# Kernel tuning notes

Hardware: AMD Instinct MI355X
Metric: run time of the kernel (lower is better)

The kernel has to match this reference:

```python
import jax, jax.numpy as jnp
import numpy as np

N, E, G = 50000, 800000, 64
IN, H, C = 128, 3, 64
HC = H * C


def _conv(x, src, dst, Wq, bq, Wk, bk, Wv, bv, Ws, bs, Wb):
    # node-level projections, then per-edge gather
    q = (x @ Wq + bq).reshape(-1, H, C)[dst]   # [E,H,C]
    k = (x @ Wk + bk).reshape(-1, H, C)[src]
    v = (x @ Wv + bv).reshape(-1, H, C)[src]
    alpha = (q * k).sum(-1) / jnp.sqrt(jnp.float32(C))  # [E,H]
    # segment softmax over incoming edges of each target node
    amax = jax.ops.segment_max(alpha, dst, num_segments=N)
    amax = jnp.where(jnp.isfinite(amax), amax, 0.0)
    ex = jnp.exp(alpha - amax[dst])
    denom = jax.ops.segment_sum(ex, dst, num_segments=N)
    a = ex / (denom[dst] + 1e-16)
    out = jax.ops.segment_sum(a[:, :, None] * v, dst, num_segments=N).reshape(-1, HC)
    # gated skip (beta=True, root_weight=True)
    r = x @ Ws + bs
    beta = jax.nn.sigmoid(jnp.concatenate([out, r, out - r], -1) @ Wb)  # [N,1]
    return beta * r + (1.0 - beta) * out


def setup_inputs() -> dict:
    key = jax.random.key(0)
    ks = jax.random.split(key, 32)
    x = jax.random.normal(ks[0], (N, IN), dtype=jnp.float32)
    edge_index = jax.random.randint(ks[1], (2, E), 0, N, dtype=jnp.int32)
    batch = jnp.sort(jax.random.randint(ks[2], (N,), 0, G, dtype=jnp.int32))
    s = 0.05
    def w(k, shape):
        return jax.random.normal(k, shape, dtype=jnp.float32) * s
    d = {"x": x, "edge_index": edge_index, "batch": batch}
    ins = [IN, HC]
    ki = 3
    for l in range(2):
        din = ins[l]
        d[f"Wq{l}"] = w(ks[ki], (din, HC)); ki += 1
        d[f"bq{l}"] = jnp.zeros((HC,), jnp.float32)
        d[f"Wk{l}"] = w(ks[ki], (din, HC)); ki += 1
        d[f"bk{l}"] = jnp.zeros((HC,), jnp.float32)
        d[f"Wv{l}"] = w(ks[ki], (din, HC)); ki += 1
        d[f"bv{l}"] = jnp.zeros((HC,), jnp.float32)
        d[f"Ws{l}"] = w(ks[ki], (din, HC)); ki += 1
        d[f"bs{l}"] = jnp.zeros((HC,), jnp.float32)
        d[f"Wb{l}"] = w(ks[ki], (3 * HC, 1)); ki += 1
    d["Wlin"] = w(ks[ki], (HC, 1)); ki += 1
    d["blin"] = jnp.zeros((1,), jnp.float32)
    return d


def reference(x, edge_index, batch,
              Wq0, bq0, Wk0, bk0, Wv0, bv0, Ws0, bs0, Wb0,
              Wq1, bq1, Wk1, bk1, Wv1, bv1, Ws1, bs1, Wb1,
              Wlin, blin):
    src, dst = edge_index[0], edge_index[1]
    h = _conv(x, src, dst, Wq0, bq0, Wk0, bk0, Wv0, bv0, Ws0, bs0, Wb0)
    h = jax.nn.elu(h)
    h = _conv(h, src, dst, Wq1, bq1, Wk1, bk1, Wv1, bv1, Ws1, bs1, Wb1)
    h = jax.nn.elu(h)
    # global mean pool over graphs
    cnt = jax.ops.segment_sum(jnp.ones((N,), jnp.float32), batch, num_segments=G)
    pooled = jax.ops.segment_sum(h, batch, num_segments=G) / jnp.maximum(cnt, 1.0)[:, None]
    logits = (pooled @ Wlin + blin).squeeze(-1)  # [G]
    return logits
```

## Files before the change

kernel.cpp:

```cpp
#include <hip/hip_runtime.h>
#include <math.h>

#define NNODES 50000
#define NEDGES 800000
#define NGRAPH 64
#define DIM_IN 128
#define HCDIM  192
#define QKVRW  768

typedef __attribute__((ext_vector_type(8))) short short8;
typedef __attribute__((ext_vector_type(4))) float f32x4;
typedef __attribute__((ext_vector_type(2))) float f32x2;

__device__ __forceinline__ unsigned short f2bf(float f){
  unsigned int u = __float_as_uint(f);
  unsigned int r = (u + 0x7fffu + ((u>>16)&1u)) >> 16;
  return (unsigned short)r;
}

__device__ __forceinline__ float4 bf4_to_f4(uint2 u){
  float4 f;
  f.x = __uint_as_float(u.x<<16);
  f.y = __uint_as_float(u.x & 0xffff0000u);
  f.z = __uint_as_float(u.y<<16);
  f.w = __uint_as_float(u.y & 0xffff0000u);
  return f;
}

__device__ __forceinline__ float4 fp8x4_to_f4(unsigned int u){
  f32x2 lo = __builtin_amdgcn_cvt_pk_f32_fp8((int)u, false);
  f32x2 hi = __builtin_amdgcn_cvt_pk_f32_fp8((int)u, true);
  float4 f; f.x=lo[0]; f.y=lo[1]; f.z=hi[0]; f.w=hi[1];
  return f;
}

__device__ __forceinline__ float wave_sum(float v){
#pragma unroll
  for(int off=32; off>0; off>>=1) v += __shfl_xor(v, off, 64);
  return v;
}

__global__ void zero2_k(int* a, int* b, int n){
  int i = blockIdx.x*blockDim.x + threadIdx.x;
  if(i<n){ a[i]=0; b[i]=0; }
}

__global__ void hist_k(const int* __restrict__ dst, int* __restrict__ counts, int E){
  int e = blockIdx.x*blockDim.x + threadIdx.x;
  if(e<E) atomicAdd(&counts[dst[e]], 1);
}

__global__ void scan_partial(const int* __restrict__ counts, int* __restrict__ bsum, int N){
  __shared__ int lds[256];
  int t = threadIdx.x;
  int idx = blockIdx.x*256 + t;
  int v = (idx<N)? counts[idx] : 0;
  lds[t]=v; __syncthreads();
#pragma unroll
  for(int off=128; off>0; off>>=1){
    if(t<off) lds[t]+=lds[t+off];
    __syncthreads();
  }
  if(t==0) bsum[blockIdx.x]=lds[0];
}

__global__ void scan_bsum(int* bsum, int nb){
  __shared__ int lds[1024];
  int t=threadIdx.x;
  int v=(t<nb)?bsum[t]:0;
  lds[t]=v; __syncthreads();
  int x=v;
#pragma unroll
  for(int off=1; off<1024; off<<=1){
    int y=(t>=off)?lds[t-off]:0;
    __syncthreads();
    x+=y; lds[t]=x;
    __syncthreads();
  }
  if(t<nb) bsum[t]=x-v;
}

__global__ void scan_final(const int* __restrict__ counts, const int* __restrict__ bsum,
                           int* __restrict__ row_ptr, int N){
  __shared__ int lds[256];
  int t=threadIdx.x;
  int idx=blockIdx.x*256+t;
  int v=(idx<N)?counts[idx]:0;
  lds[t]=v; __syncthreads();
  int x=v;
#pragma unroll
  for(int off=1; off<256; off<<=1){
    int y=(t>=off)?lds[t-off]:0;
    __syncthreads();
    x+=y; lds[t]=x;
    __syncthreads();
  }
  if(idx<=N) row_ptr[idx]= bsum[blockIdx.x]+x-v;
}

__global__ void fill_k(const int* __restrict__ src, const int* __restrict__ dst,
                       const int* __restrict__ row_ptr, int* __restrict__ cursor,
                       int* __restrict__ csr_src, int E){
  int e = blockIdx.x*blockDim.x + threadIdx.x;
  if(e<E){
    int d = dst[e];
    int pos = row_ptr[d] + atomicAdd(&cursor[d], 1);
    csr_src[pos] = src[e];
  }
}

#define CAST_BLKS (NNODES*DIM_IN/4/256)
__global__ void prep0_k(const float* __restrict__ X, unsigned short* __restrict__ Xb,
                        const float* __restrict__ Wq, const float* __restrict__ Wk,
                        const float* __restrict__ Wv, const float* __restrict__ Ws,
                        const float* __restrict__ bq, const float* __restrict__ bk,
                        const float* __restrict__ bv, const float* __restrict__ bs,
                        unsigned short* __restrict__ Wt, float* __restrict__ bcat){
  if(blockIdx.x < CAST_BLKS){
    int i4 = (blockIdx.x*256 + threadIdx.x)*4;
    float4 v = *(const float4*)(X+i4);
    ushort4 o; o.x=f2bf(v.x); o.y=f2bf(v.y); o.z=f2bf(v.z); o.w=f2bf(v.w);
    *(ushort4*)(Xb+i4) = o;
  } else {
    int idx = (blockIdx.x-CAST_BLKS)*256 + threadIdx.x;
    if(idx < QKVRW*DIM_IN){
      int c = idx / DIM_IN, k = idx % DIM_IN;
      int mat = c/HCDIM, cm = c%HCDIM;
      const float* W = (mat==0)?Wq:(mat==1)?Wk:(mat==2)?Wv:Ws;
      Wt[(size_t)c*DIM_IN + k] = f2bf(W[(size_t)k*HCDIM + cm]);
    }
    if(idx < QKVRW){
      int mat = idx/HCDIM, cm = idx%HCDIM;
      const float* b = (mat==0)?bq:(mat==1)?bk:(mat==2)?bv:bs;
      bcat[idx] = b[cm];
    }
  }
}

__global__ void build_wt(const float* __restrict__ Wq, const float* __restrict__ Wk,
                         const float* __restrict__ Wv, const float* __restrict__ Ws,
                         const float* __restrict__ bq, const float* __restrict__ bk,
                         const float* __restrict__ bv, const float* __restrict__ bs,
                         unsigned short* __restrict__ Wt, float* __restrict__ bcat, int K){
  int idx = blockIdx.x*256 + threadIdx.x;
  if(idx < QKVRW*K){
    int c = idx / K, k = idx % K;
    int mat = c/HCDIM, cm = c%HCDIM;
    const float* W = (mat==0)?Wq:(mat==1)?Wk:(mat==2)?Wv:Ws;
    Wt[(size_t)c*K + k] = f2bf(W[(size_t)k*HCDIM + cm]);
  }
  if(idx < QKVRW){
    int mat = idx/HCDIM, cm = idx%HCDIM;
    const float* b = (mat==0)?bq:(mat==1)?bk:(mat==2)?bv:bs;
    bcat[idx] = b[cm];
  }
}

template<int K>
__global__ __launch_bounds__(256) void gemm_mfma(
    const unsigned short* __restrict__ Xb,
    const unsigned short* __restrict__ Wt,
    const float* __restrict__ bcat,
    unsigned short* __restrict__ QR,
    unsigned char* __restrict__ KV, int N)
{
  __shared__ unsigned short As[128*64];
  __shared__ unsigned short Bs[64*64];
  const int tid = threadIdx.x;
  const int wv = tid>>6;
  const int lane = tid&63;
  const int m0  = blockIdx.x*128;
  const int cb  = blockIdx.y;
  const int mat = cb/3;
  const int nc0 = cb*64;

  const int wr = wv>>1, wc = wv&1;
  const int lhi = lane>>4, llo = lane&15;
  f32x4 acc[4][2] = {};

  constexpr int NT = K/64;
#pragma unroll
  for(int kt=0; kt<NT; ++kt){
    if(kt>0) __syncthreads();
#pragma unroll
    for(int it=0; it<4; ++it){
      int p = it*256 + tid;
      int r = p>>3, c = p&7;
      int cs = c ^ (r&7);
      int grow = m0 + r; if(grow > N-1) grow = N-1;
      const unsigned short* gp = Xb + (size_t)grow*K + kt*64 + cs*8;
      unsigned short* lp = As + (size_t)(it*256 + wv*64)*8;
      __builtin_amdgcn_global_load_lds(
          (const __attribute__((address_space(1))) unsigned int*)gp,
          (__attribute__((address_space(3))) unsigned int*)lp, 16, 0, 0);
    }
#pragma unroll
    for(int it=0; it<2; ++it){
      int p = it*256 + tid;
      int r = p>>3, c = p&7;
      int cs = c ^ (r&7);
      const unsigned short* gp = Wt + (size_t)(nc0 + r)*K + kt*64 + cs*8;
      unsigned short* lp = Bs + (size_t)(it*256 + wv*64)*8;
      __builtin_amdgcn_global_load_lds(
          (const __attribute__((address_space(1))) unsigned int*)gp,
          (__attribute__((address_space(3))) unsigned int*)lp, 16, 0, 0);
    }
    __syncthreads();

#pragma unroll
    for(int kk=0; kk<64; kk+=32){
      short8 a[4], b[2];
      const int chunk = (kk>>3) + lhi;
#pragma unroll
      for(int i=0;i<4;++i){
        int rr = wr*64 + i*16 + llo;
        int cs = chunk ^ (rr&7);
        a[i] = *(const short8*)(As + rr*64 + cs*8);
      }
#pragma unroll
      for(int j=0;j<2;++j){
        int cc = wc*32 + j*16 + llo;
        int cs = chunk ^ (cc&7);
        b[j] = *(const short8*)(Bs + cc*64 + cs*8);
      }
#pragma unroll
      for(int i=0;i<4;++i)
#pragma unroll
        for(int j=0;j<2;++j)
          acc[i][j] = __builtin_amdgcn_mfma_f32_16x16x32_bf16(a[i], b[j], acc[i][j], 0,0,0);
    }
  }

  const int col0 = nc0 + wc*32 + llo;
  float bias0 = bcat[col0];
  float bias1 = bcat[col0+16];
  if(mat==0 || mat==3){
    const int coff = (mat==0) ? col0 : col0-384;
#pragma unroll
    for(int i=0;i<4;++i){
#pragma unroll
      for(int r=0;r<4;++r){
        int grow = m0 + wr*64 + i*16 + lhi*4 + r;
        if(grow < N){
          size_t base = (size_t)grow*384 + coff;
          QR[base]      = f2bf(acc[i][0][r] + bias0);
          QR[base + 16] = f2bf(acc[i][1][r] + bias1);
        }
      }
    }
  } else {
#pragma unroll
    for(int i=0;i<4;++i){
#pragma unroll
      for(int r=0;r<4;++r){
        int grow = m0 + wr*64 + i*16 + lhi*4 + r;
        float v0 = acc[i][0][r] + bias0;
        float v1 = acc[i][1][r] + bias1;
        float n0 = __shfl_xor(v0, 1, 64);
        float n1 = __shfl_xor(v1, 1, 64);
        if(((llo&1)==0) && grow < N){
          int p0 = __builtin_amdgcn_cvt_pk_fp8_f32(v0, n0, 0, false);
          int p1 = __builtin_amdgcn_cvt_pk_fp8_f32(v1, n1, 0, false);
          unsigned char* kb = KV + (size_t)grow*384 + (col0-192);
          *(unsigned short*)(kb)    = (unsigned short)(p0 & 0xffff);
          *(unsigned short*)(kb+16) = (unsigned short)(p1 & 0xffff);
        }
      }
    }
  }
}

template<bool OUTBF>
__global__ __launch_bounds__(256) void attn_kernel(
  const unsigned short* __restrict__ QR,
  const unsigned char* __restrict__ KV,
  const int* __restrict__ row_ptr, const int* __restrict__ csr_src,
  const float* __restrict__ Wb, float* __restrict__ HoutF,
  unsigned short* __restrict__ HoutB, int N)
{
  const int wave = threadIdx.x>>6;
  const int lane = threadIdx.x&63;
  const int g    = lane>>4;
  const int l    = lane&15;
  const int n = blockIdx.x*4 + wave;
  if(n>=N) return;

  const unsigned short* nr = QR + (size_t)n*384 + 4*l;
  float4 q0 = bf4_to_f4(*(const uint2*)(nr));
  float4 q1 = bf4_to_f4(*(const uint2*)(nr+64));
  float4 q2 = bf4_to_f4(*(const uint2*)(nr+128));

  const int s0 = row_ptr[n];
  const int deg = row_ptr[n+1]-s0;

  float4 a0={0,0,0,0}, a1={0,0,0,0}, a2={0,0,0,0};
  float d0=0.f,d1=0.f,d2=0.f;

  unsigned int ku0=0,ku1=0,ku2=0,vu0=0,vu1=0,vu2=0;
  if(deg>0){
    int i0 = s0 + (g<deg ? g : 0); if(i0 > NEDGES-1) i0 = NEDGES-1;
    int sCur = csr_src[i0];
    const unsigned int* kv = (const unsigned int*)(KV + (size_t)sCur*384) + l;
    ku0=kv[0]; ku1=kv[16]; ku2=kv[32]; vu0=kv[48]; vu1=kv[64]; vu2=kv[80];
  }
  for(int base=0; base<deg; base+=4){
    const int inext = base + 4 + g;
    const int sNxt = csr_src[s0 + (inext<deg ? inext : 0)];
    const unsigned int* kvN = (const unsigned int*)(KV + (size_t)sNxt*384) + l;
    unsigned int nk0=kvN[0], nk1=kvN[16], nk2=kvN[32];
    unsigned int nv0=kvN[48], nv1=kvN[64], nv2=kvN[80];

    const bool valid = (base + g < deg);
    float4 k0 = fp8x4_to_f4(ku0);
    float4 k1 = fp8x4_to_f4(ku1);
    float4 k2 = fp8x4_to_f4(ku2);
    float p0 = q0.x*k0.x+q0.y*k0.y+q0.z*k0.z+q0.w*k0.w;
    float p1 = q1.x*k1.x+q1.y*k1.y+q1.z*k1.z+q1.w*k1.w;
    float p2 = q2.x*k2.x+q2.y*k2.y+q2.z*k2.z+q2.w*k2.w;
#pragma unroll
    for(int off=1; off<16; off<<=1){
      p0 += __shfl_xor(p0, off, 64);
      p1 += __shfl_xor(p1, off, 64);
      p2 += __shfl_xor(p2, off, 64);
    }
    float e0 = valid ? __expf(0.125f*p0) : 0.f;
    float e1 = valid ? __expf(0.125f*p1) : 0.f;
    float e2 = valid ? __expf(0.125f*p2) : 0.f;
    d0 += e0; d1 += e1; d2 += e2;
    float4 v0 = fp8x4_to_f4(vu0);
    float4 v1 = fp8x4_to_f4(vu1);
    float4 v2 = fp8x4_to_f4(vu2);
    a0.x+=e0*v0.x; a0.y+=e0*v0.y; a0.z+=e0*v0.z; a0.w+=e0*v0.w;
    a1.x+=e1*v1.x; a1.y+=e1*v1.y; a1.z+=e1*v1.z; a1.w+=e1*v1.w;
    a2.x+=e2*v2.x; a2.y+=e2*v2.y; a2.z+=e2*v2.z; a2.w+=e2*v2.w;

    ku0=nk0; ku1=nk1; ku2=nk2; vu0=nv0; vu1=nv1; vu2=nv2;
  }

#pragma unroll
  for(int off=16; off<64; off<<=1){
    a0.x+=__shfl_xor(a0.x,off,64); a0.y+=__shfl_xor(a0.y,off,64);
    a0.z+=__shfl_xor(a0.z,off,64); a0.w+=__shfl_xor(a0.w,off,64);
    a1.x+=__shfl_xor(a1.x,off,64); a1.y+=__shfl_xor(a1.y,off,64);
    a1.z+=__shfl_xor(a1.z,off,64); a1.w+=__shfl_xor(a1.w,off,64);
    a2.x+=__shfl_xor(a2.x,off,64); a2.y+=__shfl_xor(a2.y,off,64);
    a2.z+=__shfl_xor(a2.z,off,64); a2.w+=__shfl_xor(a2.w,off,64);
    d0+=__shfl_xor(d0,off,64); d1+=__shfl_xor(d1,off,64); d2+=__shfl_xor(d2,off,64);
  }
  const float id0=1.f/(d0+1e-16f), id1=1.f/(d1+1e-16f), id2=1.f/(d2+1e-16f);
  float4 o0, o1, o2;
  o0.x=a0.x*id0; o0.y=a0.y*id0; o0.z=a0.z*id0; o0.w=a0.w*id0;
  o1.x=a1.x*id1; o1.y=a1.y*id1; o1.z=a1.z*id1; o1.w=a1.w*id1;
  o2.x=a2.x*id2; o2.y=a2.y*id2; o2.z=a2.z*id2; o2.w=a2.w*id2;

  float4 r0 = bf4_to_f4(*(const uint2*)(nr+192));
  float4 r1 = bf4_to_f4(*(const uint2*)(nr+256));
  float4 r2 = bf4_to_f4(*(const uint2*)(nr+320));

  const float* wb = Wb + 4*l;
  float4 w00=*(const float4*)(wb),     w01=*(const float4*)(wb+64),  w02=*(const float4*)(wb+128);
  float4 w10=*(const float4*)(wb+192), w11=*(const float4*)(wb+256), w12=*(const float4*)(wb+320);
  float4 w20=*(const float4*)(wb+384), w21=*(const float4*)(wb+448), w22=*(const float4*)(wb+512);
  float z =
    o0.x*w00.x+o0.y*w00.y+o0.z*w00.z+o0.w*w00.w +
    o1.x*w01.x+o1.y*w01.y+o1.z*w01.z+o1.w*w01.w +
    o2.x*w02.x+o2.y*w02.y+o2.z*w02.z+o2.w*w02.w +
    r0.x*w10.x+r0.y*w10.y+r0.z*w10.z+r0.w*w10.w +
    r1.x*w11.x+r1.y*w11.y+r1.z*w11.z+r1.w*w11.w +
    r2.x*w12.x+r2.y*w12.y+r2.z*w12.z+r2.w*w12.w +
    (o0.x-r0.x)*w20.x+(o0.y-r0.y)*w20.y+(o0.z-r0.z)*w20.z+(o0.w-r0.w)*w20.w +
    (o1.x-r1.x)*w21.x+(o1.y-r1.y)*w21.y+(o1.z-r1.z)*w21.z+(o1.w-r1.w)*w21.w +
    (o2.x-r2.x)*w22.x+(o2.y-r2.y)*w22.y+(o2.z-r2.z)*w22.z+(o2.w-r2.w)*w22.w;
#pragma unroll
  for(int off=1; off<16; off<<=1) z += __shfl_xor(z, off, 64);
  const float beta = 1.f/(1.f+__expf(-z));
  float4 h0,h1,h2;
  h0.x=beta*r0.x+(1.f-beta)*o0.x; h0.y=beta*r0.y+(1.f-beta)*o0.y;
  h0.z=beta*r0.z+(1.f-beta)*o0.z; h0.w=beta*r0.w+(1.f-beta)*o0.w;
  h1.x=beta*r1.x+(1.f-beta)*o1.x; h1.y=beta*r1.y+(1.f-beta)*o1.y;
  h1.z=beta*r1.z+(1.f-beta)*o1.z; h1.w=beta*r1.w+(1.f-beta)*o1.w;
  h2.x=beta*r2.x+(1.f-beta)*o2.x; h2.y=beta*r2.y+(1.f-beta)*o2.y;
  h2.z=beta*r2.z+(1.f-beta)*o2.z; h2.w=beta*r2.w+(1.f-beta)*o2.w;
  h0.x=(h0.x>0.f)?h0.x:expm1f(h0.x); h0.y=(h0.y>0.f)?h0.y:expm1f(h0.y);
  h0.z=(h0.z>0.f)?h0.z:expm1f(h0.z); h0.w=(h0.w>0.f)?h0.w:expm1f(h0.w);
  h1.x=(h1.x>0.f)?h1.x:expm1f(h1.x); h1.y=(h1.y>0.f)?h1.y:expm1f(h1.y);
  h1.z=(h1.z>0.f)?h1.z:expm1f(h1.z); h1.w=(h1.w>0.f)?h1.w:expm1f(h1.w);
  h2.x=(h2.x>0.f)?h2.x:expm1f(h2.x); h2.y=(h2.y>0.f)?h2.y:expm1f(h2.y);
  h2.z=(h2.z>0.f)?h2.z:expm1f(h2.z); h2.w=(h2.w>0.f)?h2.w:expm1f(h2.w);
  if(g==0){
    if(OUTBF){
      unsigned short* hb = HoutB + (size_t)n*HCDIM + 4*l;
      ushort4 u0, u1, u2;
      u0.x=f2bf(h0.x); u0.y=f2bf(h0.y); u0.z=f2bf(h0.z); u0.w=f2bf(h0.w);
      u1.x=f2bf(h1.x); u1.y=f2bf(h1.y); u1.z=f2bf(h1.z); u1.w=f2bf(h1.w);
      u2.x=f2bf(h2.x); u2.y=f2bf(h2.y); u2.z=f2bf(h2.z); u2.w=f2bf(h2.w);
      *(ushort4*)(hb)     = u0;
      *(ushort4*)(hb+64)  = u1;
      *(ushort4*)(hb+128) = u2;
    } else {
      float* ho = HoutF + (size_t)n*HCDIM + 4*l;
      *(float4*)(ho)     = h0;
      *(float4*)(ho+64)  = h1;
      *(float4*)(ho+128) = h2;
    }
  }
}

__global__ void zero_pool(float* pooled, int* cnt){
  int i = blockIdx.x*256 + threadIdx.x;
  if(i < NGRAPH*HCDIM) ((int*)pooled)[i]=0;
  if(i < NGRAPH) cnt[i]=0;
}

__global__ void pool_k(const float* __restrict__ H, const int* __restrict__ batch,
                       float* __restrict__ pooled, int* __restrict__ cnt, int N){
  const int t = threadIdx.x;
  int start = blockIdx.x*256;
  int end = min(start+256, N);
  if(start>=N) return;
  int cur = batch[start];
  float acc = 0.f;
  int run = 0;
  for(int nn=start; nn<end; ++nn){
    int g = batch[nn];
    if(g!=cur){
      atomicAdd(&pooled[(size_t)cur*HCDIM+t], acc);
      if(t==0) atomicAdd(&cnt[cur], run);
      acc=0.f; run=0; cur=g;
    }
    acc += H[(size_t)nn*HCDIM+t];
    run++;
  }
  atomicAdd(&pooled[(size_t)cur*HCDIM+t], acc);
  if(t==0) atomicAdd(&cnt[cur], run);
}

__global__ void logits_k(const float* __restrict__ pooled, const int* __restrict__ cnt,
                         const float* __restrict__ Wlin, const float* __restrict__ blin,
                         float* __restrict__ out){
  const int g = blockIdx.x;
  const int lane = threadIdx.x;
  float c = fmaxf((float)cnt[g], 1.f);
  float s = 0.f;
#pragma unroll
  for(int j=0;j<3;++j){
    int col = j*64+lane;
    s += pooled[(size_t)g*HCDIM+col]/c * Wlin[col];
  }
  s = wave_sum(s);
  if(lane==0) out[g] = s + blin[0];
}

extern "C" void kernel_launch(void* const* d_in, const int* in_sizes, int n_in,
                              void* d_out, int out_size, void* d_ws, size_t ws_size,
                              hipStream_t stream)
{
  const int N=NNODES, E=NEDGES;
  const float* x     = (const float*)d_in[0];
  const int*   ei    = (const int*)d_in[1];
  const int*   batch = (const int*)d_in[2];
  const int* esrc = ei;
  const int* edst = ei + E;
  const float* Wq0=(const float*)d_in[3];  const float* bq0=(const float*)d_in[4];
  const float* Wk0=(const float*)d_in[5];  const float* bk0=(const float*)d_in[6];
  const float* Wv0=(const float*)d_in[7];  const float* bv0=(const float*)d_in[8];
  const float* Ws0=(const float*)d_in[9];  const float* bs0=(const float*)d_in[10];
  const float* Wb0=(const float*)d_in[11];
  const float* Wq1=(const float*)d_in[12]; const float* bq1=(const float*)d_in[13];
  const float* Wk1=(const float*)d_in[14]; const float* bk1=(const float*)d_in[15];
  const float* Wv1=(const float*)d_in[16]; const float* bv1=(const float*)d_in[17];
  const float* Ws1=(const float*)d_in[18]; const float* bs1=(const float*)d_in[19];
  const float* Wb1=(const float*)d_in[20];
  const float* Wlin=(const float*)d_in[21];
  const float* blin=(const float*)d_in[22];
  float* out = (float*)d_out;

  char* p = (char*)d_ws;
  auto alloc = [&](size_t bytes)->char*{
    char* q = p; p += (bytes+255)/256*256; return q;
  };
  unsigned short* Xb   = (unsigned short*)alloc((size_t)N*HCDIM*2);
  unsigned short* QR   = (unsigned short*)alloc((size_t)N*384*2);
  unsigned char*  KV   = (unsigned char*)alloc((size_t)N*384);
  float* H1            = (float*)alloc((size_t)N*HCDIM*4);
  unsigned short* Wt   = (unsigned short*)alloc((size_t)QKVRW*HCDIM*2);
  float* bcat          = (float*)alloc(QKVRW*4);
  int* counts  = (int*)alloc((size_t)N*4);
  int* cursor  = (int*)alloc((size_t)N*4);
  int* row_ptr = (int*)alloc((size_t)(N+1)*4);
  int* csr     = (int*)alloc((size_t)E*4);
  int* bsum    = (int*)alloc(4096);
  float* pooled= (float*)alloc((size_t)NGRAPH*HCDIM*4);
  int* cnt     = (int*)alloc(256);

  const int NB = (N+255)/256;

  zero2_k<<<(N+255)/256,256,0,stream>>>(counts,cursor,N);
  hist_k<<<(E+255)/256,256,0,stream>>>(edst,counts,E);
  scan_partial<<<NB,256,0,stream>>>(counts,bsum,N);
  scan_bsum<<<1,1024,0,stream>>>(bsum,NB);
  scan_final<<<NB,256,0,stream>>>(counts,bsum,row_ptr,N);
  fill_k<<<(E+255)/256,256,0,stream>>>(esrc,edst,row_ptr,cursor,csr,E);

  dim3 ggemm((N+127)/128, 12);
  prep0_k<<<CAST_BLKS + (QKVRW*DIM_IN+255)/256, 256, 0, stream>>>(
      x, Xb, Wq0,Wk0,Wv0,Ws0, bq0,bk0,bv0,bs0, Wt, bcat);
  gemm_mfma<DIM_IN><<<ggemm,256,0,stream>>>(Xb,Wt,bcat,QR,KV,N);
  attn_kernel<true><<<(N+3)/4,256,0,stream>>>(QR,KV,row_ptr,csr,Wb0,nullptr,Xb,N);
  build_wt<<<(QKVRW*HCDIM+255)/256,256,0,stream>>>(Wq1,Wk1,Wv1,Ws1,bq1,bk1,bv1,bs1,Wt,bcat,HCDIM);
  gemm_mfma<HCDIM><<<ggemm,256,0,stream>>>(Xb,Wt,bcat,QR,KV,N);
  attn_kernel<false><<<(N+3)/4,256,0,stream>>>(QR,KV,row_ptr,csr,Wb1,H1,nullptr,N);

  zero_pool<<<(NGRAPH*HCDIM+255)/256,256,0,stream>>>(pooled,cnt);
  pool_k<<<(N+255)/256,192,0,stream>>>(H1,batch,pooled,cnt,N);
  logits_k<<<NGRAPH,64,0,stream>>>(pooled,cnt,Wlin,blin,out);
}
```

Before: 406.1 us.

## Widen GEMM column tile to 128 and reorder weight blocks Q,S,K,V

The fused QKVS projection GEMM now computes 128x128 output tiles instead of 128x64, halving the grid's column dimension and doubling per-wave accumulators. This halves re-reads of the activation tile per output. Weight and bias blocks are reordered to Q,S,K,V so each 128-column tile writes either only the bf16 Q/R buffer or only the fp8 K/V buffer. The cost is more registers and LDS per block, which may lower occupancy, plus fewer blocks to spread across the GPU.

After: 408.5 us. No clear change (+0.6%).

```diff
diff --git a/kernel.cpp b/kernel.cpp
--- a/kernel.cpp
+++ b/kernel.cpp
@@ -126,12 +126,12 @@
     if(idx < QKVRW*DIM_IN){
       int c = idx / DIM_IN, k = idx % DIM_IN;
       int mat = c/HCDIM, cm = c%HCDIM;
-      const float* W = (mat==0)?Wq:(mat==1)?Wk:(mat==2)?Wv:Ws;
+      const float* W = (mat==0)?Wq:(mat==1)?Ws:(mat==2)?Wk:Wv;
       Wt[(size_t)c*DIM_IN + k] = f2bf(W[(size_t)k*HCDIM + cm]);
     }
     if(idx < QKVRW){
       int mat = idx/HCDIM, cm = idx%HCDIM;
-      const float* b = (mat==0)?bq:(mat==1)?bk:(mat==2)?bv:bs;
+      const float* b = (mat==0)?bq:(mat==1)?bs:(mat==2)?bk:bv;
       bcat[idx] = b[cm];
     }
   }
@@ -146,12 +146,12 @@
   if(idx < QKVRW*K){
     int c = idx / K, k = idx % K;
     int mat = c/HCDIM, cm = c%HCDIM;
-    const float* W = (mat==0)?Wq:(mat==1)?Wk:(mat==2)?Wv:Ws;
+    const float* W = (mat==0)?Wq:(mat==1)?Ws:(mat==2)?Wk:Wv;
     Wt[(size_t)c*K + k] = f2bf(W[(size_t)k*HCDIM + cm]);
   }
   if(idx < QKVRW){
     int mat = idx/HCDIM, cm = idx%HCDIM;
-    const float* b = (mat==0)?bq:(mat==1)?bk:(mat==2)?bv:bs;
+    const float* b = (mat==0)?bq:(mat==1)?bs:(mat==2)?bk:bv;
     bcat[idx] = b[cm];
   }
 }
@@ -165,18 +165,16 @@
     unsigned char* __restrict__ KV, int N)
 {
   __shared__ unsigned short As[128*64];
-  __shared__ unsigned short Bs[64*64];
+  __shared__ unsigned short Bs[128*64];
   const int tid = threadIdx.x;
   const int wv = tid>>6;
   const int lane = tid&63;
   const int m0  = blockIdx.x*128;
-  const int cb  = blockIdx.y;
-  const int mat = cb/3;
-  const int nc0 = cb*64;
+  const int nc0 = blockIdx.y*128;
 
   const int wr = wv>>1, wc = wv&1;
   const int lhi = lane>>4, llo = lane&15;
-  f32x4 acc[4][2] = {};
+  f32x4 acc[4][4] = {};
 
   constexpr int NT = K/64;
 #pragma unroll
@@ -195,7 +193,7 @@
           (__attribute__((address_space(3))) unsigned int*)lp, 16, 0, 0);
     }
 #pragma unroll
-    for(int it=0; it<2; ++it){
+    for(int it=0; it<4; ++it){
       int p = it*256 + tid;
       int r = p>>3, c = p&7;
       int cs = c ^ (r&7);
@@ -209,7 +207,7 @@
 
 #pragma unroll
     for(int kk=0; kk<64; kk+=32){
-      short8 a[4], b[2];
+      short8 a[4], b[4];
       const int chunk = (kk>>3) + lhi;
 #pragma unroll
       for(int i=0;i<4;++i){
@@ -218,52 +216,49 @@
         a[i] = *(const short8*)(As + rr*64 + cs*8);
       }
 #pragma unroll
-      for(int j=0;j<2;++j){
-        int cc = wc*32 + j*16 + llo;
+      for(int j=0;j<4;++j){
+        int cc = wc*64 + j*16 + llo;
         int cs = chunk ^ (cc&7);
         b[j] = *(const short8*)(Bs + cc*64 + cs*8);
       }
 #pragma unroll
       for(int i=0;i<4;++i)
 #pragma unroll
-        for(int j=0;j<2;++j)
+        for(int j=0;j<4;++j)
           acc[i][j] = __builtin_amdgcn_mfma_f32_16x16x32_bf16(a[i], b[j], acc[i][j], 0,0,0);
     }
   }
 
-  const int col0 = nc0 + wc*32 + llo;
-  float bias0 = bcat[col0];
-  float bias1 = bcat[col0+16];
-  if(mat==0 || mat==3){
-    const int coff = (mat==0) ? col0 : col0-384;
-#pragma unroll
-    for(int i=0;i<4;++i){
-#pragma unroll
-      for(int r=0;r<4;++r){
-        int grow = m0 + wr*64 + i*16 + lhi*4 + r;
-        if(grow < N){
-          size_t base = (size_t)grow*384 + coff;
-          QR[base]      = f2bf(acc[i][0][r] + bias0);
-          QR[base + 16] = f2bf(acc[i][1][r] + bias1);
+  if(nc0 < 384){
+#pragma unroll
+    for(int j=0;j<4;++j){
+      const int col = nc0 + wc*64 + j*16 + llo;
+      const float bias = bcat[col];
+#pragma unroll
+      for(int i=0;i<4;++i){
+#pragma unroll
+        for(int r=0;r<4;++r){
+          int grow = m0 + wr*64 + i*16 + lhi*4 + r;
+          if(grow < N) QR[(size_t)grow*384 + col] = f2bf(acc[i][j][r] + bias);
         }
       }
     }
   } else {
 #pragma unroll
-    for(int i=0;i<4;++i){
-#pragma unroll
-      for(int r=0;r<4;++r){
-        int grow = m0 + wr*64 + i*16 + lhi*4 + r;
-        float v0 = acc[i][0][r] + bias0;
-        float v1 = acc[i][1][r] + bias1;
-        float n0 = __shfl_xor(v0, 1, 64);
-        float n1 = __shfl_xor(v1, 1, 64);
-        if(((llo&1)==0) && grow < N){
-          int p0 = __builtin_amdgcn_cvt_pk_fp8_f32(v0, n0, 0, false);
-          int p1 = __builtin_amdgcn_cvt_pk_fp8_f32(v1, n1, 0, false);
-          unsigned char* kb = KV + (size_t)grow*384 + (col0-192);
-          *(unsigned short*)(kb)    = (unsigned short)(p0 & 0xffff);
-          *(unsigned short*)(kb+16) = (unsigned short)(p1 & 0xffff);
+    for(int j=0;j<4;++j){
+      const int col = nc0 - 384 + wc*64 + j*16 + llo;
+      const float bias = bcat[col + 384];
+#pragma unroll
+      for(int i=0;i<4;++i){
+#pragma unroll
+        for(int r=0;r<4;++r){
+          int grow = m0 + wr*64 + i*16 + lhi*4 + r;
+          float v0 = acc[i][j][r] + bias;
+          float n0 = __shfl_xor(v0, 1, 64);
+          if(((llo&1)==0) && grow < N){
+            int p0 = __builtin_amdgcn_cvt_pk_fp8_f32(v0, n0, 0, false);
+            *(unsigned short*)(KV + (size_t)grow*384 + col) = (unsigned short)(p0 & 0xffff);
+          }
         }
       }
     }
@@ -502,7 +497,7 @@
   scan_final<<<NB,256,0,stream>>>(counts,bsum,row_ptr,N);
   fill_k<<<(E+255)/256,256,0,stream>>>(esrc,edst,row_ptr,cursor,csr,E);
 
-  dim3 ggemm((N+127)/128, 12);
+  dim3 ggemm((N+127)/128, 6);
   prep0_k<<<CAST_BLKS + (QKVRW*DIM_IN+255)/256, 256, 0, stream>>>(
       x, Xb, Wq0,Wk0,Wv0,Ws0, bq0,bk0,bv0,bs0, Wt, bcat);
   gemm_mfma<DIM_IN><<<ggemm,256,0,stream>>>(Xb,Wt,bcat,QR,KV,N);
```
